# Performance work log

Hardware: AMD Instinct MI355X
Metric: run time of the kernel (lower is better)

Reference implementation:

```python
import jax, jax.numpy as jnp
import numpy as np


def setup_inputs() -> dict:
    key = jax.random.key(0)
    kW, kH, kT = jax.random.split(key, 3)
    N, rank, M = 1024, 8, 4096
    W = jax.random.normal(kW, (N, rank), dtype=jnp.float32)
    H = jax.random.normal(kH, (rank, M), dtype=jnp.float32)
    tau = jax.random.normal(kT, (N, rank), dtype=jnp.float32)
    return {"W": W, "H": H, "tau": tau}


def reference(W, H, tau):
    # W: [N, rank] float, H: [rank, M] float, tau: [N, rank] float
    M = H.shape[1]
    Nf = M // 2 + 1
    # FFT of nonneg-constrained H, keep first Nf bins, rebuild full Hermitian spectrum
    Hf = jnp.fft.fft(jax.nn.softplus(H), axis=1)[:, :Nf]            # [rank, Nf]
    Hf_rev = Hf[:, 1:Nf - 1][:, ::-1]                               # [rank, M - Nf]
    Hft = jnp.concatenate([Hf, jnp.conj(Hf_rev)], axis=1)           # [rank, M]
    f = jnp.arange(M, dtype=jnp.float32) / M                        # [M]
    # phase shift per (sample, component, freq): omega = exp(-i 2 pi tau f)
    omega = jnp.exp((-2j * jnp.pi) * (tau[:, :, None] * f))         # [N, rank, M] complex64
    Wp = jax.nn.softplus(W).astype(omega.dtype)                     # [N, rank]
    # fused: V[N,M] = sum_d softplus(W)[N,d] * omega[N,d,M] * Hft[d,M]
    V = jnp.einsum('Nd,NdM,dM->NM', Wp, omega, Hft)
    return V
```

## Files before the change

### kernel.cpp

```cpp
#include <hip/hip_runtime.h>
#include <math.h>

#define N_ROWS 1024
#define RANK   8
#define M_COLS 4096

#define R_ROWS   2
#define T_PTS    2
#define M_STRIDE 1024

__device__ float2 g_Hft[RANK * M_COLS];
__device__ float4 g_Tab4[N_ROWS * RANK];
__device__ float2 g_Tab2[N_ROWS * RANK];

__device__ __forceinline__ float softplus_f(float x) {
    float t = __expf(x);
    float r = 0.69314718056f * __log2f(1.0f + t);
    return (x > 20.0f) ? x : r;
}
__device__ __forceinline__ float sin_rev(float x) { return __builtin_amdgcn_sinf(x); }
__device__ __forceinline__ float cos_rev(float x) { return __builtin_amdgcn_cosf(x); }
__device__ __forceinline__ float fract_f(float x) { return __builtin_amdgcn_fractf(x); }
__device__ __forceinline__ float rfl(float x) {
    return __int_as_float(__builtin_amdgcn_readfirstlane(__float_as_int(x)));
}

__global__ void fft_fused(const float* __restrict__ H,
                          const float* __restrict__ W,
                          const float* __restrict__ tau) {
    __shared__ float  sHs[M_COLS];
    __shared__ float2 sY[4 * 64];

    int tid = threadIdx.x;
    int d   = blockIdx.x >> 4;
    int m0b = (blockIdx.x & 15) << 2;

    if (blockIdx.x < 32) {
        int t = blockIdx.x * 256 + tid;
        float w  = softplus_f(W[t]);
        float tv = tau[t];
        float rv = fract_f(tv * ((float)M_STRIDE / (float)M_COLS));
        float4 t4;
        t4.x = cos_rev(rv);
        t4.y = sin_rev(rv);
        float rc = fract_f(-tv);
        t4.z = w * cos_rev(rc);
        t4.w = w * sin_rev(rc);
        g_Tab4[t] = t4;
        g_Tab2[t] = make_float2(w, tv);
    }

    const float4* Hrow4 = (const float4*)(H + d * M_COLS);
    #pragma unroll
    for (int p = 0; p < 4; ++p) {
        int i = p * 256 + tid;
        float4 h4 = Hrow4[i];
        sHs[i*4+0] = softplus_f(h4.x);
        sHs[i*4+1] = softplus_f(h4.y);
        sHs[i*4+2] = softplus_f(h4.z);
        sHs[i*4+3] = softplus_f(h4.w);
    }
    __syncthreads();

    {
        int k0 = tid & 63, j = tid >> 6;
        int m0 = m0b + j;
        float mrev = (float)m0 * (1.0f / 64.0f);
        float rr =  cos_rev(mrev);
        float ri = -sin_rev(mrev);
        float twr = 1.0f, twi = 0.0f;
        float ar = 0.0f, ai = 0.0f;
        #pragma unroll
        for (int k1 = 0; k1 < 64; ++k1) {
            float v = sHs[(k1 << 6) + k0];
            ar = fmaf(v, twr, ar);
            ai = fmaf(v, twi, ai);
            float nr = fmaf(twr, rr, -(twi * ri));
            twi      = fmaf(twr, ri,   twi * rr);
            twr = nr;
        }
        sY[(j << 6) + k0] = make_float2(ar, ai);
    }
    __syncthreads();

    {
        int m1 = tid & 63, j = tid >> 6;
        int m  = (m1 << 6) + m0b + j;
        float mrev = (float)m * (1.0f / 4096.0f);
        float rr =  cos_rev(mrev);
        float ri = -sin_rev(mrev);
        float twr = 1.0f, twi = 0.0f;
        float ar = 0.0f, ai = 0.0f;
        #pragma unroll
        for (int k0 = 0; k0 < 64; ++k0) {
            float2 y = sY[(j << 6) + k0];
            ar = fmaf(y.x, twr, fmaf(-y.y, twi, ar));
            ai = fmaf(y.x, twi, fmaf( y.y, twr, ai));
            float nr = fmaf(twr, rr, -(twi * ri));
            twi      = fmaf(twr, ri,   twi * rr);
            twr = nr;
        }
        g_Hft[d * M_COLS + m] = make_float2(ar, ai);
    }
}

__global__ void shiftnmf_main(float* __restrict__ out) {
    int tid = threadIdx.x;
    int m0  = blockIdx.x * 256 + tid;
    int n0  = blockIdx.y * R_ROWS;

    float fm0 = (float)(1 + m0) * (1.0f / (float)M_COLS);

    float accm[R_ROWS][T_PTS];
    float accx[R_ROWS][T_PTS];
    #pragma unroll
    for (int r = 0; r < R_ROWS; ++r)
        #pragma unroll
        for (int j = 0; j < T_PTS; ++j) { accm[r][j] = 0.0f; accx[r][j] = 0.0f; }

    #pragma unroll
    for (int d = 0; d < RANK; ++d) {
        float ur[R_ROWS], ui[R_ROWS];
        float vr[R_ROWS], vi[R_ROWS];
        float ws[R_ROWS], wcr[R_ROWS], wci[R_ROWS];
        #pragma unroll
        for (int r = 0; r < R_ROWS; ++r) {
            int nd = (n0 + r) * RANK + d;
            float4 t4 = g_Tab4[nd];
            float2 t2 = g_Tab2[nd];
            vr[r]  = rfl(t4.x);  vi[r]  = rfl(t4.y);
            wcr[r] = rfl(t4.z);  wci[r] = rfl(t4.w);
            ws[r]  = rfl(t2.x);
            float tv = rfl(t2.y);
            float r0 = fract_f(tv * fm0);
            ur[r] = cos_rev(r0);
            ui[r] = sin_rev(r0);
        }

        const float2* hp = g_Hft + d * M_COLS + 1 + m0;
        #pragma unroll
        for (int j = 0; j < T_PTS; ++j) {
            float2 h = hp[j * M_STRIDE];
            #pragma unroll
            for (int r = 0; r < R_ROWS; ++r) {
                float t1 = ui[r] * h.y;
                float zr = fmaf(ur[r], h.x, t1);
                float t2v = ui[r] * h.x;
                float zi = fmaf(ur[r], h.y, -t2v);
                accm[r][j] = fmaf(ws[r],  zr, accm[r][j]);
                accx[r][j] = fmaf(wcr[r], zr, fmaf(wci[r], zi, accx[r][j]));
                if (j < T_PTS - 1) {
                    float nr = fmaf(ur[r], vr[r], -(ui[r] * vi[r]));
                    ui[r]    = fmaf(ur[r], vi[r],   ui[r] * vr[r]);
                    ur[r]    = nr;
                }
            }
        }
    }

    #pragma unroll
    for (int r = 0; r < R_ROWS; ++r) {
        float* op = out + (n0 + r) * M_COLS;
        #pragma unroll
        for (int j = 0; j < T_PTS; ++j)
            op[1 + m0 + j * M_STRIDE] = accm[r][j];
        #pragma unroll
        for (int j = 0; j < T_PTS; ++j)
            op[4095 - m0 - j * M_STRIDE] = accx[r][j];
    }

    if (blockIdx.x == 0 && tid == 0) {
        #pragma unroll
        for (int r = 0; r < R_ROWS; ++r) {
            int n = n0 + r;
            float a = 0.0f;
            #pragma unroll
            for (int d = 0; d < RANK; ++d)
                a = fmaf(g_Tab2[n * RANK + d].x, g_Hft[d * M_COLS].x, a);
            out[n * M_COLS] = a;
        }
    }
}

extern "C" void kernel_launch(void* const* d_in, const int* in_sizes, int n_in,
                              void* d_out, int out_size, void* d_ws, size_t ws_size,
                              hipStream_t stream) {
    const float* W   = (const float*)d_in[0];
    const float* H   = (const float*)d_in[1];
    const float* tau = (const float*)d_in[2];

    fft_fused<<<dim3(RANK * 16), dim3(256), 0, stream>>>(H, W, tau);

    dim3 grid(M_COLS / 2 / (256 * T_PTS), N_ROWS / R_ROWS);
    shiftnmf_main<<<grid, dim3(256), 0, stream>>>((float*)d_out);
}
```

Measured before the change: 19.20 us.

## Precompute factored phase tables to replace per-element sincos in main kernel

Splits the phase exp(-2πi·tau·(1+m)/M) into two precomputed factors: a per-(n,d) table over the low 6 bits of m (64 entries) and one over 16 coarse steps. The extra blocks added to the FFT kernel fill these tables, and the main kernel combines them with a complex multiply instead of calling sin/cos. This removes transcendental work from the hot loop. In exchange it adds about 5 MB of table writes and per-thread gathered reads in the main kernel.

```diff
diff --git a/kernel.cpp b/kernel.cpp
--- a/kernel.cpp
+++ b/kernel.cpp
@@ -12,6 +12,8 @@
 __device__ float2 g_Hft[RANK * M_COLS];
 __device__ float4 g_Tab4[N_ROWS * RANK];
 __device__ float2 g_Tab2[N_ROWS * RANK];
+__device__ float2 g_T1[N_ROWS * RANK * 64];
+__device__ float2 g_T2[N_ROWS * RANK * 16];
 
 __device__ __forceinline__ float softplus_f(float x) {
     float t = __expf(x);
@@ -28,10 +30,31 @@
 __global__ void fft_fused(const float* __restrict__ H,
                           const float* __restrict__ W,
                           const float* __restrict__ tau) {
+    int tid = threadIdx.x;
+
+    if (blockIdx.x >= 128) {
+        int b = blockIdx.x - 128;
+        if (b < 2048) {
+            int idx = b * 256 + tid;
+            int nd  = idx >> 6;
+            int l   = idx & 63;
+            float tv  = tau[nd];
+            float rev = fract_f(tv * ((float)l * (1.0f / (float)M_COLS)));
+            g_T1[idx] = make_float2(cos_rev(rev), sin_rev(rev));
+        } else {
+            int idx = (b - 2048) * 256 + tid;
+            int nd  = idx >> 4;
+            int q   = idx & 15;
+            float tv  = tau[nd];
+            float rev = fract_f(tv * ((float)(64 * q + 1) * (1.0f / (float)M_COLS)));
+            g_T2[idx] = make_float2(cos_rev(rev), sin_rev(rev));
+        }
+        return;
+    }
+
     __shared__ float  sHs[M_COLS];
     __shared__ float2 sY[4 * 64];
 
-    int tid = threadIdx.x;
     int d   = blockIdx.x >> 4;
     int m0b = (blockIdx.x & 15) << 2;
 
@@ -108,8 +131,8 @@
     int tid = threadIdx.x;
     int m0  = blockIdx.x * 256 + tid;
     int n0  = blockIdx.y * R_ROWS;
-
-    float fm0 = (float)(1 + m0) * (1.0f / (float)M_COLS);
+    int l   = tid & 63;
+    int q   = (m0 >> 6) & 15;
 
     float accm[R_ROWS][T_PTS];
     float accx[R_ROWS][T_PTS];
@@ -127,14 +150,14 @@
         for (int r = 0; r < R_ROWS; ++r) {
             int nd = (n0 + r) * RANK + d;
             float4 t4 = g_Tab4[nd];
-            float2 t2 = g_Tab2[nd];
             vr[r]  = rfl(t4.x);  vi[r]  = rfl(t4.y);
             wcr[r] = rfl(t4.z);  wci[r] = rfl(t4.w);
-            ws[r]  = rfl(t2.x);
-            float tv = rfl(t2.y);
-            float r0 = fract_f(tv * fm0);
-            ur[r] = cos_rev(r0);
-            ui[r] = sin_rev(r0);
+            ws[r]  = rfl(g_Tab2[nd].x);
+            float2 t2 = g_T2[nd * 16 + q];
+            float t2r = rfl(t2.x), t2i = rfl(t2.y);
+            float2 t1 = g_T1[nd * 64 + l];
+            ur[r] = fmaf(t1.x, t2r, -(t1.y * t2i));
+            ui[r] = fmaf(t1.x, t2i,   t1.y * t2r);
         }
 
         const float2* hp = g_Hft + d * M_COLS + 1 + m0;
@@ -143,8 +166,8 @@
             float2 h = hp[j * M_STRIDE];
             #pragma unroll
             for (int r = 0; r < R_ROWS; ++r) {
-                float t1 = ui[r] * h.y;
-                float zr = fmaf(ur[r], h.x, t1);
+                float t1v = ui[r] * h.y;
+                float zr = fmaf(ur[r], h.x, t1v);
                 float t2v = ui[r] * h.x;
                 float zi = fmaf(ur[r], h.y, -t2v);
                 accm[r][j] = fmaf(ws[r],  zr, accm[r][j]);
@@ -189,7 +212,7 @@
     const float* H   = (const float*)d_in[1];
     const float* tau = (const float*)d_in[2];
 
-    fft_fused<<<dim3(RANK * 16), dim3(256), 0, stream>>>(H, W, tau);
+    fft_fused<<<dim3(128 + 2048 + 512), dim3(256), 0, stream>>>(H, W, tau);
 
     dim3 grid(M_COLS / 2 / (256 * T_PTS), N_ROWS / R_ROWS);
     shiftnmf_main<<<grid, dim3(256), 0, stream>>>((float*)d_out);
```

Result: slower. 29.09 us (+51.5%).
